# Optimization experiments

Measured on AMD Instinct MI355X. Metric: run time of the kernel, lower is better.

## Reference

```python
import jax, jax.numpy as jnp
import numpy as np

NG = 128        # grid points per dim (hardcoded grid_size in source)
P = 4           # Gaussian spread support window per dim -> P^3 = 64 cells/atom
L = 10.0        # cubic box edge (box_vecs diagonal)
C = 32          # hidden_channels
MAXZ = 128
N = 10000       # atoms
NBATCH = 1


def setup_inputs() -> dict:
    key = jax.random.key(0)
    ks = jax.random.split(key, 8)
    z = jax.random.randint(ks[0], (N,), 0, MAXZ, dtype=jnp.int32)
    pos = jax.random.uniform(ks[1], (N, 3), dtype=jnp.float32) * L
    batch = jnp.zeros((N,), dtype=jnp.int32)
    emb = jax.random.normal(ks[2], (MAXZ, C), dtype=jnp.float32) * 0.1
    sc = 1.0 / np.sqrt(C)
    W0 = jax.random.normal(ks[3], (C, C), dtype=jnp.float32) * sc
    b0 = jax.random.normal(ks[4], (C,), dtype=jnp.float32) * 0.01
    W1 = jax.random.normal(ks[5], (C, C), dtype=jnp.float32) * sc
    b1 = jax.random.normal(ks[6], (C,), dtype=jnp.float32) * 0.01
    return {"z": z, "pos": pos, "batch": batch, "emb": emb,
            "W0": W0, "b0": b0, "W1": W1, "b1": b1}


def _window(pos, batch):
    """Gaussian spread weights [N, P^3] and flat grid indices [N, P^3] (periodic)."""
    h = L / NG                       # grid spacing
    sig = h                          # Gaussian width = one grid spacing
    pw = jnp.mod(pos, L)             # wrap into box, [N,3] (x,y,z)
    base = jnp.floor(pw / h).astype(jnp.int32)           # [N,3]
    offs = jnp.arange(P, dtype=jnp.int32) - (P // 2 - 1) # [-1,0,1,2]
    cell = base[:, :, None] + offs[None, None, :]        # [N,3,P]
    d = pw[:, :, None] - cell.astype(pw.dtype) * h       # distance to cell centers
    wd = jnp.exp(-0.5 * (d / sig) ** 2)                  # [N,3,P] per-dim weights
    # separable product -> [N, Px, Py, Pz] -> [N, P^3]
    w = (wd[:, 0, :, None, None] * wd[:, 1, None, :, None]
         * wd[:, 2, None, None, :]).reshape(pos.shape[0], -1)
    ci = jnp.mod(cell, NG)                               # periodic wrap
    ix, iy, iz = ci[:, 0], ci[:, 1], ci[:, 2]            # [N,P] each
    flat = (batch[:, None, None, None].astype(jnp.int32) * (NG ** 3)
            + iz[:, None, None, :] * (NG ** 2)
            + iy[:, None, :, None] * NG
            + ix[:, :, None, None]).reshape(pos.shape[0], -1)  # [N,P^3]
    return w, flat, sig


def _forward(z, pos, batch, emb, W0, b0, W1, b1):
    # AtomicEncoder: embedding + 2-layer MLP with silu after every linear
    x = emb[z]
    x = jax.nn.silu(x @ W0.T + b0)
    x = jax.nn.silu(x @ W1.T + b1)                       # [N,C]

    w, flat, sig = _window(pos, batch)
    # spread: scatter-add Gaussian-weighted features onto [NBATCH*NG^3, C]
    vals = w[:, :, None] * x[:, None, :]                 # [N,P^3,C]
    field = jnp.zeros((NBATCH * NG ** 3, C), dtype=x.dtype)
    field = field.at[flat.reshape(-1)].add(vals.reshape(-1, C))
    field = field.reshape(NBATCH, NG, NG, NG, C)         # (b, z, y, x, c)

    # FFT convolution with Gaussian k-space kernel
    F = jnp.fft.rfftn(field, axes=(1, 2, 3))             # [B,NG,NG,NG//2+1,C]
    h = L / NG
    kz = 2 * jnp.pi * jnp.fft.fftfreq(NG, d=h).astype(jnp.float32)
    kx = 2 * jnp.pi * jnp.fft.rfftfreq(NG, d=h).astype(jnp.float32)
    k2 = (kz[:, None, None] ** 2 + kz[None, :, None] ** 2
          + kx[None, None, :] ** 2)
    G = jnp.exp(-0.5 * sig * sig * k2)                   # [NG,NG,NG//2+1]
    e_field = jnp.fft.irfftn(F * G[None, :, :, :, None],
                             s=(NG, NG, NG), axes=(1, 2, 3))

    # interpolate: Gaussian-weighted gather back to atom positions
    g = e_field.reshape(NBATCH * NG ** 3, C)[flat]       # [N,P^3,C]
    energy = (w[:, :, None] * g).sum(axis=(1, 2))        # [N]
    return energy


def reference(z, pos, batch, emb, W0, b0, W1, b1):
    return _forward(z, pos, batch, emb, W0, b0, W1, b1)
```

## Files before the change

### kernel.cpp

```cpp
#include <hip/hip_runtime.h>
#include <math.h>

#define NGRID 128
#define CH 32
#define RADC 4
#define CBITS 3
#define NCELL 16
#define CAP 32
#define CSHIFT 5

constexpr float L_BOX = 10.0f;
constexpr float H = L_BOX / NGRID;

struct Ktaps { float k[RADC + 1]; };

__device__ __forceinline__ float silu(float v) {
    return v / (1.0f + expf(-v));
}


__global__ void __launch_bounds__(256)
prep(const int* __restrict__ z, const float* __restrict__ pos,
     const float* __restrict__ emb,
     const float* __restrict__ W0, const float* __restrict__ b0,
     const float* __restrict__ W1, const float* __restrict__ b1,
     float* __restrict__ rec, int* __restrict__ cnt, int2* __restrict__ bucket,
     int N) {
    int wave = threadIdx.x >> 6, lane = threadIdx.x & 63;
    int i0 = (blockIdx.x * 4 + wave) * 2;
    if (i0 >= N) return;
    int half = lane >> 5, lane32 = lane & 31;
    int i = i0 + half;
    bool vh = i < N;
    int ic = vh ? i : (N - 1);

    int sub = lane32;
    int zi = z[ic];
    float x = emb[zi * CH + sub];

    float acc = b0[sub];
#pragma unroll
    for (int k = 0; k < CH; ++k)
        acc = fmaf(__shfl(x, k, 32), W0[sub * CH + k], acc);
    float h1 = silu(acc);

    acc = b1[sub];
#pragma unroll
    for (int k = 0; k < CH; ++k)
        acc = fmaf(__shfl(h1, k, 32), W1[sub * CH + k], acc);
    float s = silu(acc);
#pragma unroll
    for (int m = 16; m >= 1; m >>= 1) s += __shfl_xor(s, m, 32);

    float pwx = fmodf(pos[ic * 3 + 0], L_BOX);
    float pwy = fmodf(pos[ic * 3 + 1], L_BOX);
    float pwz = fmodf(pos[ic * 3 + 2], L_BOX);
    int bx = (int)floorf(pwx / H);
    int by = (int)floorf(pwy / H);
    int bz = (int)floorf(pwz / H);
    int cpv = bx | (by << 8) | (bz << 16);

    int axis = lane32 >> 2, p = lane32 & 3;
    float pwa = (axis == 0) ? pwx : ((axis == 1) ? pwy : pwz);
    int   ba  = (axis == 0) ? bx  : ((axis == 1) ? by  : bz);
    int c = ba + p - 1;
    float d = (pwa - (float)c * H) / H;
    float w = expf(-0.5f * d * d);

    float val = (lane32 < 12) ? w
              : (lane32 == 12) ? s
              : (lane32 == 13) ? __int_as_float(cpv) : 0.0f;
    if (vh && lane32 < 16) rec[i * 16 + lane32] = val;
    if (vh && lane32 == 0) {
        int cell = ((bz >> CBITS) << 8) | ((by >> CBITS) << 4) | (bx >> CBITS);
        int slot = atomicAdd(&cnt[cell], 1);
        if (slot < CAP) bucket[(cell << CSHIFT) + slot] = make_int2(cpv, i);
    }
}

__device__ __forceinline__ float axis_factor(float4 wi, float4 wj, int db,
                                             const float* __restrict__ Kl) {
    float A0 = wi.x * wj.w;
    float A1 = wi.x * wj.z + wi.y * wj.w;
    float A2 = wi.x * wj.y + wi.y * wj.z + wi.z * wj.w;
    float A3 = wi.x * wj.x + wi.y * wj.y + wi.z * wj.z + wi.w * wj.w;
    float A4 = wi.y * wj.x + wi.z * wj.y + wi.w * wj.z;
    float A5 = wi.z * wj.x + wi.w * wj.y;
    float A6 = wi.w * wj.x;
    float f;
    f  = A0 * Kl[abs(db - 3)];
    f += A1 * Kl[abs(db - 2)];
    f += A2 * Kl[abs(db - 1)];
    f += A3 * Kl[abs(db)];
    f += A4 * Kl[abs(db + 1)];
    f += A5 * Kl[abs(db + 2)];
    f += A6 * Kl[abs(db + 3)];
    return f;
}

__device__ __forceinline__ float hit_term(int idx, const float4* __restrict__ rec4,
                                          int bxi, int byi, int bzi,
                                          float4 a0, float4 a1, float4 a2,
                                          const float* __restrict__ Kl) {
    float4 b0 = rec4[idx * 4 + 0];
    float4 b1 = rec4[idx * 4 + 1];
    float4 b2 = rec4[idx * 4 + 2];
    float4 b3 = rec4[idx * 4 + 3];
    int cpj = __float_as_int(b3.y);
    int dx = (((bxi - (cpj & 127)) + 7) & 127) - 7;
    int dy = (((byi - ((cpj >> 8) & 127)) + 7) & 127) - 7;
    int dz = (((bzi - ((cpj >> 16) & 127)) + 7) & 127) - 7;
    float fx = axis_factor(a0, b0, dx, Kl);
    float fy = axis_factor(a1, b1, dy, Kl);
    float fz = axis_factor(a2, b2, dz, Kl);
    return b3.x * fx * fy * fz;
}

__global__ void __launch_bounds__(256)
pair_energy(const float* __restrict__ rec, const int* __restrict__ cnt,
            const int2* __restrict__ bucket,
            float* __restrict__ out, Ktaps K, int N) {
    __shared__ float Kl[16];
    __shared__ int hitbuf[4][128];
    int tid = threadIdx.x;
    if (tid < 16) Kl[tid] = (tid <= RADC) ? K.k[tid] : 0.0f;
    __syncthreads();

    int wave = tid >> 6, lane = tid & 63;
    int i = blockIdx.x * 4 + wave;
    bool valid = i < N;
    int ii = valid ? i : 0;

    const float4* rec4 = (const float4*)rec;
    float4 a0 = rec4[ii * 4 + 0];
    float4 a1 = rec4[ii * 4 + 1];
    float4 a2 = rec4[ii * 4 + 2];
    float4 a3 = rec4[ii * 4 + 3];
    int cpi = __float_as_int(a3.y);
    int bxi = cpi & 127, byi = (cpi >> 8) & 127, bzi = (cpi >> 16) & 127;
    int cbx = bxi >> CBITS, cby = byi >> CBITS, cbz = bzi >> CBITS;

    int k = lane;
    int ox = k % 3 - 1, oy = (k / 3) % 3 - 1, oz = k / 9 - 1;
    int cell = (((cbz + oz) & (NCELL - 1)) << 8)
             | (((cby + oy) & (NCELL - 1)) << 4)
             |  ((cbx + ox) & (NCELL - 1));
    int c = 0;
    if (lane < 27) c = min(cnt[cell], CAP);
    int cbase = cell << CSHIFT;

    int incl = c;
#pragma unroll
    for (int d = 1; d < 32; d <<= 1) {
        int v = __shfl_up(incl, d, 32);
        if ((lane & 31) >= d) incl += v;
    }
    int excl = incl - c;
    int T = __shfl(incl, 26, 64);

    int* hb = hitbuf[wave];
    int nh = 0;
    float e = 0.0f;

    for (int g0 = 0; g0 < T; g0 += 64) {
        int g = g0 + lane;
        int lo = 0;
#pragma unroll
        for (int step = 16; step >= 1; step >>= 1) {
            int nk = lo + step;
            int nkc = (nk < 27) ? nk : 26;
            int ov = __shfl(excl, nkc, 64);
            if (nk < 27 && ov <= g) lo = nk;
        }
        int off = __shfl(excl, lo, 64);
        int bas = __shfl(cbase, lo, 64);
        int slot = g - off;
        int2 ent = bucket[bas + min(slot, CAP - 1)];
        int cpj = ent.x;
        int dx = ((bxi - (cpj & 127)) + 7) & 127;
        int dy = ((byi - ((cpj >> 8) & 127)) + 7) & 127;
        int dz = ((bzi - ((cpj >> 16) & 127)) + 7) & 127;
        bool pass = (g < T) && (max(dx, max(dy, dz)) <= 14);
        unsigned long long mask = __ballot(pass);
        int myoff = __popcll(mask & ((1ull << lane) - 1ull));
        if (pass) hb[nh + myoff] = ent.y;
        __builtin_amdgcn_wave_barrier();
        nh += (int)__popcll(mask);
        if (nh >= 64) {
            e += hit_term(hb[lane], rec4, bxi, byi, bzi, a0, a1, a2, Kl);
            nh -= 64;
            __builtin_amdgcn_wave_barrier();
            int mv = (lane < nh) ? hb[64 + lane] : 0;
            __builtin_amdgcn_wave_barrier();
            if (lane < nh) hb[lane] = mv;
            __builtin_amdgcn_wave_barrier();
        }
    }
    if (lane < nh)
        e += hit_term(hb[lane], rec4, bxi, byi, bzi, a0, a1, a2, Kl);

#pragma unroll
    for (int m2 = 32; m2 >= 1; m2 >>= 1) e += __shfl_xor(e, m2, 64);
    if (valid && lane == 0) out[i] = e;
}

extern "C" void kernel_launch(void* const* d_in, const int* in_sizes, int n_in,
                              void* d_out, int out_size, void* d_ws, size_t ws_size,
                              hipStream_t stream) {
    const int*   z   = (const int*)d_in[0];
    const float* pos = (const float*)d_in[1];
    const float* emb = (const float*)d_in[3];
    const float* W0  = (const float*)d_in[4];
    const float* b0  = (const float*)d_in[5];
    const float* W1  = (const float*)d_in[6];
    const float* b1  = (const float*)d_in[7];
    int N = in_sizes[0];

    float* rec    = (float*)d_ws;
    int*   cnt    = (int*)(rec + (size_t)N * 16);
    int2*  bucket = (int2*)(cnt + 4096);

    Ktaps K;
    for (int r = 0; r <= RADC; ++r) {
        double acc = 0.0;
        for (int j = 0; j < NGRID; ++j) {
            int jj = (j < NGRID / 2) ? j : j - NGRID;
            double arg = (2.0 * M_PI * jj) / NGRID;
            acc += exp(-0.5 * arg * arg) * cos((2.0 * M_PI) * ((double)(j * r) / NGRID));
        }
        K.k[r] = (float)(acc / NGRID);
    }

    hipMemsetAsync(cnt, 0, 4096 * sizeof(int), stream);
    prep<<<(N + 7) / 8, 256, 0, stream>>>(z, pos, emb, W0, b0, W1, b1,
                                          rec, cnt, bucket, N);
    pair_energy<<<(N + 3) / 4, 256, 0, stream>>>(rec, cnt, bucket,
                                                 (float*)d_out, K, N);
}
```

Measured before the change: 90.01 us.

## Precompute per-element MLP scalar table and scatter atoms one-thread-per-atom

The per-atom embedding MLP depends only on atomic number, so it is now evaluated once for each of the 128 element types in a small setup kernel that also zeroes the cell counters, replacing the memset. A new scatter kernel handles one atom per thread, looks up the scalar, computes the twelve spread weights and writes the record as float4 stores before binning. This removes the redundant per-atom 32x32 matmuls and the memset launch, but adds a dependent launch that does little work.

```diff
diff --git a/kernel.cpp b/kernel.cpp
--- a/kernel.cpp
+++ b/kernel.cpp
@@ -3,6 +3,7 @@
 
 #define NGRID 128
 #define CH 32
+#define MAXZ 128
 #define RADC 4
 #define CBITS 3
 #define NCELL 16
@@ -20,23 +21,19 @@
 
 
 __global__ void __launch_bounds__(256)
-prep(const int* __restrict__ z, const float* __restrict__ pos,
-     const float* __restrict__ emb,
-     const float* __restrict__ W0, const float* __restrict__ b0,
-     const float* __restrict__ W1, const float* __restrict__ b1,
-     float* __restrict__ rec, int* __restrict__ cnt, int2* __restrict__ bucket,
-     int N) {
-    int wave = threadIdx.x >> 6, lane = threadIdx.x & 63;
-    int i0 = (blockIdx.x * 4 + wave) * 2;
-    if (i0 >= N) return;
+setup(const float* __restrict__ emb,
+      const float* __restrict__ W0, const float* __restrict__ b0,
+      const float* __restrict__ W1, const float* __restrict__ b1,
+      int* __restrict__ cnt, float* __restrict__ sTab) {
+    int tid = threadIdx.x;
+    cnt[blockIdx.x * 256 + tid] = 0;
+
+    int wave = tid >> 6, lane = tid & 63;
     int half = lane >> 5, lane32 = lane & 31;
-    int i = i0 + half;
-    bool vh = i < N;
-    int ic = vh ? i : (N - 1);
-
+    int zv = (blockIdx.x * 4 + wave) * 2 + half;
+    if (zv >= MAXZ) return;
     int sub = lane32;
-    int zi = z[ic];
-    float x = emb[zi * CH + sub];
+    float x = emb[zv * CH + sub];
 
     float acc = b0[sub];
 #pragma unroll
@@ -52,30 +49,49 @@
 #pragma unroll
     for (int m = 16; m >= 1; m >>= 1) s += __shfl_xor(s, m, 32);
 
-    float pwx = fmodf(pos[ic * 3 + 0], L_BOX);
-    float pwy = fmodf(pos[ic * 3 + 1], L_BOX);
-    float pwz = fmodf(pos[ic * 3 + 2], L_BOX);
-    int bx = (int)floorf(pwx / H);
-    int by = (int)floorf(pwy / H);
-    int bz = (int)floorf(pwz / H);
+    if (lane32 == 0) sTab[zv] = s;
+}
+
+__global__ void __launch_bounds__(256)
+scatter(const int* __restrict__ z, const float* __restrict__ pos,
+        const float* __restrict__ sTab,
+        float* __restrict__ rec, int* __restrict__ cnt, int2* __restrict__ bucket,
+        int N) {
+    int i = blockIdx.x * 256 + threadIdx.x;
+    if (i >= N) return;
+    float s = sTab[z[i]];
+
+    float pwx = fmodf(pos[i * 3 + 0], L_BOX);
+    float pwy = fmodf(pos[i * 3 + 1], L_BOX);
+    float pwz = fmodf(pos[i * 3 + 2], L_BOX);
+
+    float pw[3] = {pwx, pwy, pwz};
+    int   b[3];
+    float w[12];
+#pragma unroll
+    for (int axis = 0; axis < 3; ++axis) {
+        float pwa = pw[axis];
+        int ba = (int)floorf(pwa / H);
+        b[axis] = ba;
+#pragma unroll
+        for (int p = 0; p < 4; ++p) {
+            int c = ba + p - 1;
+            float d = (pwa - (float)c * H) / H;
+            w[axis * 4 + p] = expf(-0.5f * d * d);
+        }
+    }
+    int bx = b[0], by = b[1], bz = b[2];
     int cpv = bx | (by << 8) | (bz << 16);
 
-    int axis = lane32 >> 2, p = lane32 & 3;
-    float pwa = (axis == 0) ? pwx : ((axis == 1) ? pwy : pwz);
-    int   ba  = (axis == 0) ? bx  : ((axis == 1) ? by  : bz);
-    int c = ba + p - 1;
-    float d = (pwa - (float)c * H) / H;
-    float w = expf(-0.5f * d * d);
-
-    float val = (lane32 < 12) ? w
-              : (lane32 == 12) ? s
-              : (lane32 == 13) ? __int_as_float(cpv) : 0.0f;
-    if (vh && lane32 < 16) rec[i * 16 + lane32] = val;
-    if (vh && lane32 == 0) {
-        int cell = ((bz >> CBITS) << 8) | ((by >> CBITS) << 4) | (bx >> CBITS);
-        int slot = atomicAdd(&cnt[cell], 1);
-        if (slot < CAP) bucket[(cell << CSHIFT) + slot] = make_int2(cpv, i);
-    }
+    float4* r4 = (float4*)(rec + (size_t)i * 16);
+    r4[0] = make_float4(w[0], w[1], w[2],  w[3]);
+    r4[1] = make_float4(w[4], w[5], w[6],  w[7]);
+    r4[2] = make_float4(w[8], w[9], w[10], w[11]);
+    r4[3] = make_float4(s, __int_as_float(cpv), 0.0f, 0.0f);
+
+    int cell = ((bz >> CBITS) << 8) | ((by >> CBITS) << 4) | (bx >> CBITS);
+    int slot = atomicAdd(&cnt[cell], 1);
+    if (slot < CAP) bucket[(cell << CSHIFT) + slot] = make_int2(cpv, i);
 }
 
 __device__ __forceinline__ float axis_factor(float4 wi, float4 wj, int db,
@@ -218,7 +234,8 @@
 
     float* rec    = (float*)d_ws;
     int*   cnt    = (int*)(rec + (size_t)N * 16);
-    int2*  bucket = (int2*)(cnt + 4096);
+    float* sTab   = (float*)(cnt + 4096);
+    int2*  bucket = (int2*)(sTab + 128);
 
     Ktaps K;
     for (int r = 0; r <= RADC; ++r) {
@@ -231,9 +248,8 @@
         K.k[r] = (float)(acc / NGRID);
     }
 
-    hipMemsetAsync(cnt, 0, 4096 * sizeof(int), stream);
-    prep<<<(N + 7) / 8, 256, 0, stream>>>(z, pos, emb, W0, b0, W1, b1,
-                                          rec, cnt, bucket, N);
+    setup<<<16, 256, 0, stream>>>(emb, W0, b0, W1, b1, cnt, sTab);
+    scatter<<<(N + 255) / 256, 256, 0, stream>>>(z, pos, sTab, rec, cnt, bucket, N);
     pair_energy<<<(N + 3) / 4, 256, 0, stream>>>(rec, cnt, bucket,
                                                  (float*)d_out, K, N);
 }
```

New measurement: 84.56 us. 6.0% less time.
